# Kernel optimization log

Measured on AMD Instinct MI355X. Metric: run time of the kernel, lower is better.

## Reference

```python
import jax, jax.numpy as jnp
import numpy as np

N = 50000        # nodes
E = 1600000      # edges (avg degree 32)
DIM_IN = 128
H = 4            # num_heads
D1 = 100         # gc1 per-head out dim
D2 = 20          # gc2 per-head out dim
B = 64           # graphs in the batch
EPS = 1e-5
SLOPE = 0.01     # torch leaky_relu default


def setup_inputs() -> dict:
    key = jax.random.key(0)
    ks = jax.random.split(key, 16)
    sc = lambda fan: 1.0 / np.sqrt(fan)
    inp = {
        'feat': jax.random.normal(ks[0], (N, DIM_IN), jnp.float32),
        'src': jax.random.randint(ks[1], (E,), 0, N, jnp.int32),
        'dst': jax.random.randint(ks[2], (E,), 0, N, jnp.int32),
        'graph_id': jnp.sort(jax.random.randint(ks[3], (N,), 0, B, jnp.int32)),
        # GAT layer 1: per-head fc weight [H, din, dout], attn vector [H, 2*dout]
        'W1': jax.random.normal(ks[4], (H, DIM_IN, D1), jnp.float32) * sc(DIM_IN),
        'a1': jax.random.normal(ks[5], (H, 2 * D1), jnp.float32) * sc(2 * D1),
        # GAT layer 2 (input is cat of heads: H*D1 = 400)
        'W2': jax.random.normal(ks[6], (H, H * D1, D2), jnp.float32) * sc(H * D1),
        'a2': jax.random.normal(ks[7], (H, 2 * D2), jnp.float32) * sc(2 * D2),
        # readout MLP 20 -> 128 -> 32 -> 1
        'Wf1': jax.random.normal(ks[8], (D2, 128), jnp.float32) * sc(D2),
        'bf1': jnp.zeros((128,), jnp.float32),
        'Wf2': jax.random.normal(ks[9], (128, 32), jnp.float32) * sc(128),
        'bf2': jnp.zeros((32,), jnp.float32),
        'Wf3': jax.random.normal(ks[10], (32, 1), jnp.float32) * sc(32),
        'bf3': jnp.zeros((1,), jnp.float32),
        'gamma2': jnp.ones((32,), jnp.float32),   # bn2 weight
        'beta2': jnp.zeros((32,), jnp.float32),   # bn2 bias
    }
    return inp


def _gat_heads(h, W, a, src, dst):
    """Per-head GAT: gather-attn -> segment softmax over dst mailboxes -> scatter-sum.
    Returns list of [N, dout] head outputs. Loop over H=4 heads (small fixed set)."""
    outs = []
    for i in range(W.shape[0]):
        z = h @ W[i]                               # [N, dout]
        d = z.shape[1]
        s_src = z @ a[i, :d]                       # [N] (attn split: a.[z_src,z_dst])
        s_dst = z @ a[i, d:]                       # [N]
        e = jax.nn.leaky_relu(s_src[src] + s_dst[dst], SLOPE)   # [E]
        m = jax.ops.segment_max(e, dst, num_segments=N)          # stable softmax max
        ex = jnp.exp(e - m[dst])
        den = jax.ops.segment_sum(ex, dst, num_segments=N)
        alpha = ex / den[dst]                      # [E] segment softmax
        outs.append(jax.ops.segment_sum(alpha[:, None] * z[src], dst, num_segments=N))
    return outs


def reference(feat, src, dst, graph_id, W1, a1, W2, a2,
              Wf1, bf1, Wf2, bf2, Wf3, bf3, gamma2, beta2):
    src = src.astype(jnp.int32); dst = dst.astype(jnp.int32)
    h = jax.nn.relu(jnp.concatenate(_gat_heads(feat, W1, a1, src, dst), axis=1))  # [N,400]
    h = jax.nn.relu(jnp.mean(jnp.stack(_gat_heads(h, W2, a2, src, dst), 0), 0))   # [N,20]
    # dgl.mean_nodes: per-graph mean of node features
    counts = jax.ops.segment_sum(jnp.ones((N,), h.dtype), graph_id, num_segments=B)
    hg = jax.ops.segment_sum(h, graph_id, num_segments=B) / counts[:, None]        # [B,20]
    out = jax.nn.relu(hg @ Wf1 + bf1)              # dropout = identity (eval)
    out = out @ Wf2 + bf2                          # [B,32]
    mu = jnp.mean(out, axis=0)                     # BatchNorm1d (training stats, biased var)
    var = jnp.mean((out - mu) ** 2, axis=0)
    out = jax.nn.relu(gamma2 * (out - mu) * jax.lax.rsqrt(var + EPS) + beta2)
    return out @ Wf3 + bf3                         # [B,1]
```

## Files before the change

kernel.cpp:

```cpp
#include <hip/hip_runtime.h>
#include <hip/hip_bf16.h>
#include <math.h>

#define N_NODES 50000
#define N_EDGES 1600000
#define DIN 128
#define NH 4
#define D1 100
#define D2 20
#define NB 64
#define EPS_BN 1e-5f


typedef unsigned int uint;
typedef unsigned short ushort;
typedef short short8v __attribute__((ext_vector_type(8)));
typedef float float4v __attribute__((ext_vector_type(4)));

#define Z1_ROWU 224
#define Z1_HU 52
#define Z2_ROWU 64

__device__ __forceinline__ void bf16x2_unpack(uint p, float& lo, float& hi) {
  lo = __uint_as_float(p << 16);
  hi = __uint_as_float(p & 0xffff0000u);
}

__device__ __forceinline__ ushort f2bf(float f) {
  uint u = __float_as_uint(f);
  return (ushort)((u + 0x7fffu + ((u >> 16) & 1u)) >> 16);
}

__global__ void prep_b1t(const float* __restrict__ W1, ushort* __restrict__ B1t) {
  int o = blockIdx.x * 256 + threadIdx.x;
  int h = o >> 14;
  int r = o & 16383;
  int j = r >> 7, k = r & 127;
  float v = (j < D1) ? W1[((size_t)h * DIN + k) * D1 + j] : 0.f;
  B1t[o] = f2bf(v);
}

__global__ void prep_b2t(const float* __restrict__ W2, ushort* __restrict__ B2t) {
  int idx = blockIdx.x * 256 + threadIdx.x;
  if (idx >= 80 * 416) return;
  int c = idx / 416, k = idx - c * 416;
  int h = c / D2, j = c - h * D2;
  float v = (k < NH * D1) ? W2[((size_t)h * (NH * D1) + k) * D2 + j] : 0.f;
  B2t[idx] = f2bf(v);
}

__global__ __launch_bounds__(256) void gemm1_mfma(const float* __restrict__ feat,
                                                  const ushort* __restrict__ B1t,
                                                  ushort* __restrict__ z1b) {
  __shared__ __align__(16) short As[64 * 136];
  __shared__ __align__(16) short Bs[128 * 136];
  const int row0 = blockIdx.x * 64;
  const int h = blockIdx.y;
  const int tid = threadIdx.x;
#pragma unroll
  for (int it = 0; it < 8; it++) {
    int idx = tid + it * 256;
    int r = idx >> 5, c4 = idx & 31;
    int row = row0 + r;
    float4 v = make_float4(0.f, 0.f, 0.f, 0.f);
    if (row < N_NODES) v = *reinterpret_cast<const float4*>(feat + (size_t)row * DIN + c4 * 4);
    short4 s;
    s.x = (short)f2bf(v.x); s.y = (short)f2bf(v.y);
    s.z = (short)f2bf(v.z); s.w = (short)f2bf(v.w);
    *reinterpret_cast<short4*>(&As[r * 136 + c4 * 4]) = s;
  }
  {
    const uint* bsrc = reinterpret_cast<const uint*>(B1t + (size_t)h * 16384);
#pragma unroll
    for (int it = 0; it < 32; it++) {
      int idx = tid + it * 256;
      int j = idx >> 6, kk = idx & 63;
      *reinterpret_cast<uint*>(&Bs[j * 136 + kk * 2]) = bsrc[idx];
    }
  }
  __syncthreads();
  const int wv = tid >> 6, lane = tid & 63;
  const int m = lane & 15, q = lane >> 4;
  float4v acc[8];
#pragma unroll
  for (int t = 0; t < 8; t++) acc[t] = (float4v){0.f, 0.f, 0.f, 0.f};
#pragma unroll
  for (int kq = 0; kq < 4; kq++) {
    short8v a = *reinterpret_cast<const short8v*>(&As[(wv * 16 + m) * 136 + kq * 32 + q * 8]);
#pragma unroll
    for (int t = 0; t < 8; t++) {
      short8v b = *reinterpret_cast<const short8v*>(&Bs[(t * 16 + m) * 136 + kq * 32 + q * 8]);
      acc[t] = __builtin_amdgcn_mfma_f32_16x16x32_bf16(a, b, acc[t], 0, 0, 0);
    }
  }
#pragma unroll
  for (int t = 0; t < 8; t++) {
    int cl = t * 16 + m;
    if (cl < 104) {
#pragma unroll
      for (int reg = 0; reg < 4; reg++) {
        int row = row0 + wv * 16 + q * 4 + reg;
        if (row < N_NODES)
          z1b[(size_t)row * 448 + h * 104 + cl] = (cl < D1) ? f2bf(acc[t][reg]) : (ushort)0;
      }
    }
  }
}

__global__ __launch_bounds__(256) void gemm2_mfma(const ushort* __restrict__ h1b,
                                                  const ushort* __restrict__ B2t,
                                                  ushort* __restrict__ z2b) {
  __shared__ __align__(16) short As[64 * 40];
  __shared__ __align__(16) short Bs[80 * 40];
  const int row0 = blockIdx.x * 64;
  const int tid = threadIdx.x;
  const int wv = tid >> 6, lane = tid & 63;
  const int m = lane & 15, q = lane >> 4;
  const uint* au = reinterpret_cast<const uint*>(h1b);
  const uint* bu = reinterpret_cast<const uint*>(B2t);
  uint* asu = reinterpret_cast<uint*>(As);
  uint* bsu = reinterpret_cast<uint*>(Bs);
  float4v acc[5];
#pragma unroll
  for (int t = 0; t < 5; t++) acc[t] = (float4v){0.f, 0.f, 0.f, 0.f};
  for (int ch = 0; ch < 13; ch++) {
    int k0u = ch * 16;
    {
      int idx = tid;
#pragma unroll
      for (int it = 0; it < 4; it++, idx += 256) {
        int r = idx >> 4, ku = idx & 15;
        int row = row0 + r;
        uint v = 0;
        if (row < N_NODES && (k0u + ku) < 200) v = au[(size_t)row * 200 + k0u + ku];
        asu[r * 20 + ku] = v;
      }
      idx = tid;
#pragma unroll
      for (int it = 0; it < 5; it++, idx += 256) {
        int c = idx >> 4, ku = idx & 15;
        bsu[c * 20 + ku] = bu[(size_t)c * 208 + k0u + ku];
      }
    }
    __syncthreads();
    short8v a = *reinterpret_cast<const short8v*>(&As[(wv * 16 + m) * 40 + q * 8]);
#pragma unroll
    for (int t = 0; t < 5; t++) {
      short8v b = *reinterpret_cast<const short8v*>(&Bs[(t * 16 + m) * 40 + q * 8]);
      acc[t] = __builtin_amdgcn_mfma_f32_16x16x32_bf16(a, b, acc[t], 0, 0, 0);
    }
    __syncthreads();
  }
#pragma unroll
  for (int t = 0; t < 5; t++) {
    int col = t * 16 + m;
#pragma unroll
    for (int reg = 0; reg < 4; reg++) {
      int row = row0 + wv * 16 + q * 4 + reg;
      if (row < N_NODES) z2b[(size_t)row * 128 + col] = f2bf(acc[t][reg]);
    }
  }
}

template <int DOUT, int HEADU, int ROWU>
__global__ void scores_kernel(const ushort* __restrict__ z,
                              const float* __restrict__ a,
                              float* __restrict__ ssrc,
                              float* __restrict__ sdst) {
  int t = blockIdx.x * blockDim.x + threadIdx.x;
  if (t >= N_NODES * NH) return;
  int n = t >> 2;
  int h = t & 3;
  const uint* zr = reinterpret_cast<const uint*>(z) + (size_t)n * ROWU + h * HEADU;
  const float* as = a + h * 2 * DOUT;
  const float* ad = as + DOUT;
  float s1 = 0.f, s2 = 0.f;
  for (int j = 0; j < DOUT / 2; j++) {
    float lo, hi;
    bf16x2_unpack(zr[j], lo, hi);
    s1 += lo * as[2 * j] + hi * as[2 * j + 1];
    s2 += lo * ad[2 * j] + hi * ad[2 * j + 1];
  }
  ssrc[h * N_NODES + n] = s1;
  sdst[h * N_NODES + n] = s2;
}

__global__ void hist_kernel(const int* __restrict__ dst, int* __restrict__ cnt) {
  int e = blockIdx.x * blockDim.x + threadIdx.x;
  if (e < N_EDGES) atomicAdd(&cnt[dst[e]], 1);
}

__global__ __launch_bounds__(512) void scan1_kernel(const int* __restrict__ cnt,
                                                    int* __restrict__ row_ptr,
                                                    int* __restrict__ btot, int n) {
  __shared__ int ws[8];
  int b = blockIdx.x, tid = threadIdx.x, lane = tid & 63, wv = tid >> 6;
  int i = b * 512 + tid;
  int v = (i < n) ? cnt[i] : 0;
  int orig = v;
  for (int off = 1; off < 64; off <<= 1) {
    int t = __shfl_up(v, off);
    if (lane >= off) v += t;
  }
  if (lane == 63) ws[wv] = v;
  __syncthreads();
  int wo = 0;
  for (int j = 0; j < wv; j++) wo += ws[j];
  if (i < n) row_ptr[i] = wo + v - orig;
  if (tid == 511) btot[b] = wo + v;
}

__global__ __launch_bounds__(128) void scan2_kernel(int* __restrict__ btot,
                                                    int* __restrict__ row_ptr_n, int nb) {
  __shared__ int ws2[2];
  int tid = threadIdx.x, lane = tid & 63, wv = tid >> 6;
  int v = (tid < nb) ? btot[tid] : 0;
  int orig = v;
  for (int off = 1; off < 64; off <<= 1) {
    int t = __shfl_up(v, off);
    if (lane >= off) v += t;
  }
  if (lane == 63) ws2[wv] = v;
  __syncthreads();
  int wo = (wv == 1) ? ws2[0] : 0;
  if (tid < nb) btot[tid] = wo + v - orig;
  if (tid == nb - 1) *row_ptr_n = wo + v;
}

__global__ __launch_bounds__(512) void scan3_kernel(int* __restrict__ row_ptr,
                                                    int* __restrict__ cursor,
                                                    const int* __restrict__ btot, int n) {
  int i = blockIdx.x * 512 + threadIdx.x;
  if (i < n) {
    int v = row_ptr[i] + btot[blockIdx.x];
    row_ptr[i] = v;
    cursor[i] = v;
  }
}

__global__ void fill_kernel(const int* __restrict__ src, const int* __restrict__ dst,
                            int* __restrict__ cursor, int* __restrict__ csr_src) {
  int e = blockIdx.x * blockDim.x + threadIdx.x;
  if (e < N_EDGES) {
    int p = atomicAdd(&cursor[dst[e]], 1);
    csr_src[p] = src[e];
  }
}

__global__ __launch_bounds__(256) void agg1_kernel(const ushort* __restrict__ z,
                                                   const float* __restrict__ ssrc,
                                                   const float* __restrict__ sdst,
                                                   const int* __restrict__ row_ptr,
                                                   const int* __restrict__ csr_src,
                                                   ushort* __restrict__ h1b) {
  __shared__ float lw[NH][128];
  const int d = blockIdx.x;
  const int h = threadIdx.x >> 6, lane = threadIdx.x & 63;
  const int beg = row_ptr[d], end = row_ptr[d + 1];
  const int deg = end - beg;
  uint* h1u = reinterpret_cast<uint*>(h1b);
  const size_t ou = (size_t)d * 200 + h * 50 + lane;
  const bool act = lane < D1 / 2;
  if (deg == 0) {
    if (act) h1u[ou] = 0u;
    return;
  }
  const int hN = h * N_NODES;
  const float sd = sdst[hN + d];
  const uint* zb = reinterpret_cast<const uint*>(z);
  const int hco = h * Z1_HU + lane;
  float den = 0.f;
  float aE0 = 0.f, aE1 = 0.f, aE2 = 0.f, aE3 = 0.f;
  float aO0 = 0.f, aO1 = 0.f, aO2 = 0.f, aO3 = 0.f;
  for (int c0 = 0; c0 < deg; c0 += 128) {
    const int cn = min(128, deg - c0);
    const int cb = beg + c0;
    for (int i = lane; i < cn; i += 64) {
      int s = csr_src[cb + i];
      float e = ssrc[hN + s] + sd;
      e = fmaxf(e, 0.01f * e);
      float x = __expf(e);
      lw[h][i] = x;
      den += x;
    }
    if (act) {
      int j = 0;
      for (; j + 8 <= cn; j += 8) {
        int s0 = csr_src[cb + j + 0], s1 = csr_src[cb + j + 1];
        int s2 = csr_src[cb + j + 2], s3 = csr_src[cb + j + 3];
        int s4 = csr_src[cb + j + 4], s5 = csr_src[cb + j + 5];
        int s6 = csr_src[cb + j + 6], s7 = csr_src[cb + j + 7];
        float x0 = lw[h][j + 0], x1 = lw[h][j + 1];
        float x2 = lw[h][j + 2], x3 = lw[h][j + 3];
        float x4 = lw[h][j + 4], x5 = lw[h][j + 5];
        float x6 = lw[h][j + 6], x7 = lw[h][j + 7];
        uint p0 = zb[(size_t)s0 * Z1_ROWU + hco];
        uint p1 = zb[(size_t)s1 * Z1_ROWU + hco];
        uint p2 = zb[(size_t)s2 * Z1_ROWU + hco];
        uint p3 = zb[(size_t)s3 * Z1_ROWU + hco];
        uint p4 = zb[(size_t)s4 * Z1_ROWU + hco];
        uint p5 = zb[(size_t)s5 * Z1_ROWU + hco];
        uint p6 = zb[(size_t)s6 * Z1_ROWU + hco];
        uint p7 = zb[(size_t)s7 * Z1_ROWU + hco];
        float lo, hi;
        bf16x2_unpack(p0, lo, hi); aE0 += x0 * lo; aO0 += x0 * hi;
        bf16x2_unpack(p1, lo, hi); aE1 += x1 * lo; aO1 += x1 * hi;
        bf16x2_unpack(p2, lo, hi); aE2 += x2 * lo; aO2 += x2 * hi;
        bf16x2_unpack(p3, lo, hi); aE3 += x3 * lo; aO3 += x3 * hi;
        bf16x2_unpack(p4, lo, hi); aE0 += x4 * lo; aO0 += x4 * hi;
        bf16x2_unpack(p5, lo, hi); aE1 += x5 * lo; aO1 += x5 * hi;
        bf16x2_unpack(p6, lo, hi); aE2 += x6 * lo; aO2 += x6 * hi;
        bf16x2_unpack(p7, lo, hi); aE3 += x7 * lo; aO3 += x7 * hi;
      }
      for (; j < cn; j++) {
        int s = csr_src[cb + j];
        float x = lw[h][j];
        uint p = zb[(size_t)s * Z1_ROWU + hco];
        float lo, hi;
        bf16x2_unpack(p, lo, hi);
        aE0 += x * lo;
        aO0 += x * hi;
      }
    }
  }
#pragma unroll
  for (int off = 32; off > 0; off >>= 1) den += __shfl_xor(den, off);
  if (!act) return;
  float inv = 1.0f / den;
  float vE = ((aE0 + aE1) + (aE2 + aE3)) * inv;
  float vO = ((aO0 + aO1) + (aO2 + aO3)) * inv;
  vE = vE > 0.f ? vE : 0.f;
  vO = vO > 0.f ? vO : 0.f;
  h1u[ou] = (uint)f2bf(vE) | ((uint)f2bf(vO) << 16);
}

__global__ __launch_bounds__(256) void agg2_kernel(const ushort* __restrict__ z,
                                                   const float* __restrict__ ssrc,
                                                   const float* __restrict__ sdst,
                                                   const int* __restrict__ row_ptr,
                                                   const int* __restrict__ csr_src,
                                                   float* __restrict__ h2) {
  __shared__ float xw[4][8][4];
  __shared__ int sw[4][8];
  __shared__ float accb[4][40][2];
  __shared__ float denb[4][4];
  const int d = blockIdx.x;
  const int wv = threadIdx.x >> 6, lane = threadIdx.x & 63;
  const int beg = row_ptr[d];
  const int deg = row_ptr[d + 1] - beg;
  if (deg == 0) {
    if (threadIdx.x < D2) h2[(size_t)d * D2 + threadIdx.x] = 0.f;
    return;
  }
  const int eh_h = lane & 3, eh_e = lane >> 2;
  const int hq = lane / 10;
  const uint* zu = reinterpret_cast<const uint*>(z);
  float sd = 0.f;
  if (lane < 32) sd = sdst[eh_h * N_NODES + d];
  float den = 0.f;
  float acc0 = 0.f, acc1 = 0.f;
  for (int c0 = wv * 8; c0 < deg; c0 += 32) {
    const int cn = min(8, deg - c0);
    const int cb = beg + c0;
    if (lane < 32) {
      int ee = (eh_e < cn) ? eh_e : 0;
      int s = csr_src[cb + ee];
      float e = ssrc[eh_h * N_NODES + s] + sd;
      e = fmaxf(e, 0.01f * e);
      float x = (eh_e < cn) ? __expf(e) : 0.f;
      den += x;
      xw[wv][eh_e][eh_h] = x;
      if (eh_h == 0) sw[wv][eh_e] = s;
    }
    if (lane < 40) {
#pragma unroll
      for (int e = 0; e < 8; e++) {
        int se = sw[wv][e];
        float xx = xw[wv][e][hq];
        uint p = zu[(size_t)se * Z2_ROWU + lane];
        float lo, hi;
        bf16x2_unpack(p, lo, hi);
        acc0 += xx * lo;
        acc1 += xx * hi;
      }
    }
  }
  den += __shfl_xor(den, 4);
  den += __shfl_xor(den, 8);
  den += __shfl_xor(den, 16);
  if (lane < 4) denb[wv][lane] = den;
  if (lane < 40) {
    accb[wv][lane][0] = acc0;
    accb[wv][lane][1] = acc1;
  }
  __syncthreads();
  if (threadIdx.x < 10) {
    int j = threadIdx.x;
    float vE = 0.f, vO = 0.f;
#pragma unroll
    for (int h = 0; h < 4; h++) {
      float dn = denb[0][h] + denb[1][h] + denb[2][h] + denb[3][h];
      float invd = 1.0f / dn;
      int sl = h * 10 + j;
      float lo = accb[0][sl][0] + accb[1][sl][0] + accb[2][sl][0] + accb[3][sl][0];
      float hi = accb[0][sl][1] + accb[1][sl][1] + accb[2][sl][1] + accb[3][sl][1];
      vE += lo * invd;
      vO += hi * invd;
    }
    vE *= 0.25f;
    vO *= 0.25f;
    h2[(size_t)d * D2 + 2 * j] = vE > 0.f ? vE : 0.f;
    h2[(size_t)d * D2 + 2 * j + 1] = vO > 0.f ? vO : 0.f;
  }
}

__global__ __launch_bounds__(256) void pool_kernel(const float* __restrict__ h2,
                                                   const int* __restrict__ gid,
                                                   float* __restrict__ hg,
                                                   int* __restrict__ gcnt) {
  int wave = threadIdx.x >> 6, lane = threadIdx.x & 63;
  int n = (blockIdx.x * 4 + wave) * 64 + lane;
  bool valid = n < N_NODES;
  int g = gid[valid ? n : (N_NODES - 1)];
  int g0 = __shfl(g, 0), g63 = __shfl(g, 63);
  unsigned long long mask = __ballot(valid);
  if (g0 == g63) {
    if (lane == 0) atomicAdd(&gcnt[g0], (int)__popcll(mask));
#pragma unroll
    for (int c = 0; c < D2; c++) {
      float v = valid ? h2[(size_t)n * D2 + c] : 0.f;
#pragma unroll
      for (int off = 32; off > 0; off >>= 1) v += __shfl_xor(v, off);
      if (lane == 0) atomicAdd(&hg[g0 * D2 + c], v);
    }
  } else if (valid) {
    atomicAdd(&gcnt[g], 1);
    for (int c = 0; c < D2; c++) atomicAdd(&hg[g * D2 + c], h2[(size_t)n * D2 + c]);
  }
}

__global__ __launch_bounds__(256) void head_kernel(const float* __restrict__ hg,
                                                   const int* __restrict__ gcnt,
                                                   const float* __restrict__ Wf1,
                                                   const float* __restrict__ bf1,
                                                   const float* __restrict__ Wf2,
                                                   const float* __restrict__ bf2,
                                                   const float* __restrict__ Wf3,
                                                   const float* __restrict__ bf3,
                                                   const float* __restrict__ gamma,
                                                   const float* __restrict__ beta,
                                                   float* __restrict__ out) {
  __shared__ float X[NB][D2];
  __shared__ float T1[NB][128];
  __shared__ float T2[NB][32];
  __shared__ float scale_s[32], shift_s[32];
  int tid = threadIdx.x;
  for (int i = tid; i < NB * D2; i += 256) {
    int r = i / D2, c = i % D2;
    X[r][c] = hg[i] / (float)gcnt[r];
  }
  __syncthreads();
  for (int i = tid; i < NB * 128; i += 256) {
    int r = i >> 7, c = i & 127;
    float s = bf1[c];
#pragma unroll
    for (int k = 0; k < D2; k++) s += X[r][k] * Wf1[k * 128 + c];
    T1[r][c] = s > 0.f ? s : 0.f;
  }
  __syncthreads();
  for (int i = tid; i < NB * 32; i += 256) {
    int r = i >> 5, c = i & 31;
    float s = bf2[c];
#pragma unroll
    for (int k = 0; k < 128; k++) s += T1[r][k] * Wf2[k * 32 + c];
    T2[r][c] = s;
  }
  __syncthreads();
  if (tid < 32) {
    float mu = 0.f;
    for (int r = 0; r < NB; r++) mu += T2[r][tid];
    mu *= (1.f / NB);
    float var = 0.f;
    for (int r = 0; r < NB; r++) {
      float dv = T2[r][tid] - mu;
      var += dv * dv;
    }
    var *= (1.f / NB);
    float sc = gamma[tid] * rsqrtf(var + EPS_BN);
    scale_s[tid] = sc;
    shift_s[tid] = beta[tid] - mu * sc;
  }
  __syncthreads();
  if (tid < NB) {
    float s = bf3[0];
#pragma unroll
    for (int c = 0; c < 32; c++) {
      float y = scale_s[c] * T2[tid][c] + shift_s[c];
      y = y > 0.f ? y : 0.f;
      s += y * Wf3[c];
    }
    out[tid] = s;
  }
}


extern "C" void kernel_launch(void* const* d_in, const int* in_sizes, int n_in,
                              void* d_out, int out_size, void* d_ws, size_t ws_size,
                              hipStream_t stream) {
  const float* feat = (const float*)d_in[0];
  const int* src = (const int*)d_in[1];
  const int* dst = (const int*)d_in[2];
  const int* gid = (const int*)d_in[3];
  const float* W1 = (const float*)d_in[4];
  const float* a1 = (const float*)d_in[5];
  const float* W2 = (const float*)d_in[6];
  const float* a2 = (const float*)d_in[7];
  const float* Wf1 = (const float*)d_in[8];
  const float* bf1 = (const float*)d_in[9];
  const float* Wf2 = (const float*)d_in[10];
  const float* bf2 = (const float*)d_in[11];
  const float* Wf3 = (const float*)d_in[12];
  const float* bf3 = (const float*)d_in[13];
  const float* gamma2 = (const float*)d_in[14];
  const float* beta2 = (const float*)d_in[15];
  float* outp = (float*)d_out;

  char* p = (char*)d_ws;
  auto alloc = [&](size_t bytes) {
    void* q = (void*)p;
    p += (bytes + 255) & ~(size_t)255;
    return q;
  };
  ushort* z1b = (ushort*)alloc((size_t)N_NODES * 448 * 2);
  ushort* z2b = (ushort*)alloc((size_t)N_NODES * 128 * 2);
  ushort* h1b = (ushort*)alloc((size_t)N_NODES * NH * D1 * 2);
  float* h2 = (float*)alloc((size_t)N_NODES * D2 * 4);
  float* ssrc = (float*)alloc((size_t)NH * N_NODES * 4);
  float* sdst = (float*)alloc((size_t)NH * N_NODES * 4);
  int* cnt = (int*)alloc((size_t)N_NODES * 4);
  int* row_ptr = (int*)alloc((size_t)(N_NODES + 1) * 4);
  int* cursor = (int*)alloc((size_t)N_NODES * 4);
  int* csr = (int*)alloc((size_t)N_EDGES * 4);
  int* btot = (int*)alloc((size_t)128 * 4);
  ushort* B1t = (ushort*)alloc((size_t)NH * 128 * 128 * 2);
  ushort* B2t = (ushort*)alloc((size_t)80 * 416 * 2);
  float* hg = (float*)alloc((size_t)NB * D2 * 4);
  int* gcnt = (int*)alloc((size_t)NB * 4);

  const int rows64 = (N_NODES + 63) / 64;
  const int eblk = (N_EDGES + 255) / 256;
  const int nblk = (N_NODES + 255) / 256;
  const int nhblk = (N_NODES * NH + 255) / 256;
  const int sblk = (N_NODES + 511) / 512;

  hipMemsetAsync(cnt, 0, (size_t)N_NODES * 4, stream);
  hist_kernel<<<eblk, 256, 0, stream>>>(dst, cnt);
  scan1_kernel<<<sblk, 512, 0, stream>>>(cnt, row_ptr, btot, N_NODES);
  scan2_kernel<<<1, 128, 0, stream>>>(btot, row_ptr + N_NODES, sblk);
  scan3_kernel<<<sblk, 512, 0, stream>>>(row_ptr, cursor, btot, N_NODES);
  fill_kernel<<<eblk, 256, 0, stream>>>(src, dst, cursor, csr);

  prep_b1t<<<256, 256, 0, stream>>>(W1, B1t);
  prep_b2t<<<130, 256, 0, stream>>>(W2, B2t);

  gemm1_mfma<<<dim3(rows64, NH), 256, 0, stream>>>(feat, B1t, z1b);
  scores_kernel<D1, Z1_HU, Z1_ROWU><<<nhblk, 256, 0, stream>>>(z1b, a1, ssrc, sdst);
  agg1_kernel<<<N_NODES, 256, 0, stream>>>(z1b, ssrc, sdst, row_ptr, csr, h1b);

  gemm2_mfma<<<rows64, 256, 0, stream>>>(h1b, B2t, z2b);
  scores_kernel<D2, 10, Z2_ROWU><<<nhblk, 256, 0, stream>>>(z2b, a2, ssrc, sdst);
  agg2_kernel<<<N_NODES, 256, 0, stream>>>(z2b, ssrc, sdst, row_ptr, csr, h2);

  hipMemsetAsync(hg, 0, (size_t)NB * D2 * 4, stream);
  hipMemsetAsync(gcnt, 0, (size_t)NB * 4, stream);
  pool_kernel<<<nblk, 256, 0, stream>>>(h2, gid, hg, gcnt);
  head_kernel<<<1, 256, 0, stream>>>(hg, gcnt, Wf1, bf1, Wf2, bf2, Wf3, bf3,
                                     gamma2, beta2, outp);
}
```

Baseline: 733.0 us.

## Record edge ranks in histogram, shrink z1 row stride, retile gemm1 to 128 rows

After: 631.2 us. 1.16x faster.

```diff
diff --git a/kernel.cpp b/kernel.cpp
--- a/kernel.cpp
+++ b/kernel.cpp
@@ -17,7 +17,7 @@
 typedef short short8v __attribute__((ext_vector_type(8)));
 typedef float float4v __attribute__((ext_vector_type(4)));
 
-#define Z1_ROWU 224
+#define Z1_ROWU 208
 #define Z1_HU 52
 #define Z2_ROWU 64
 
@@ -52,23 +52,10 @@
 __global__ __launch_bounds__(256) void gemm1_mfma(const float* __restrict__ feat,
                                                   const ushort* __restrict__ B1t,
                                                   ushort* __restrict__ z1b) {
-  __shared__ __align__(16) short As[64 * 136];
   __shared__ __align__(16) short Bs[128 * 136];
-  const int row0 = blockIdx.x * 64;
+  const int row0 = blockIdx.x * 128;
   const int h = blockIdx.y;
   const int tid = threadIdx.x;
-#pragma unroll
-  for (int it = 0; it < 8; it++) {
-    int idx = tid + it * 256;
-    int r = idx >> 5, c4 = idx & 31;
-    int row = row0 + r;
-    float4 v = make_float4(0.f, 0.f, 0.f, 0.f);
-    if (row < N_NODES) v = *reinterpret_cast<const float4*>(feat + (size_t)row * DIN + c4 * 4);
-    short4 s;
-    s.x = (short)f2bf(v.x); s.y = (short)f2bf(v.y);
-    s.z = (short)f2bf(v.z); s.w = (short)f2bf(v.w);
-    *reinterpret_cast<short4*>(&As[r * 136 + c4 * 4]) = s;
-  }
   {
     const uint* bsrc = reinterpret_cast<const uint*>(B1t + (size_t)h * 16384);
 #pragma unroll
@@ -78,30 +65,55 @@
       *reinterpret_cast<uint*>(&Bs[j * 136 + kk * 2]) = bsrc[idx];
     }
   }
-  __syncthreads();
   const int wv = tid >> 6, lane = tid & 63;
   const int m = lane & 15, q = lane >> 4;
-  float4v acc[8];
-#pragma unroll
-  for (int t = 0; t < 8; t++) acc[t] = (float4v){0.f, 0.f, 0.f, 0.f};
+  short8v a[2][4];
+#pragma unroll
+  for (int mt = 0; mt < 2; mt++) {
+    int row = row0 + wv * 32 + mt * 16 + m;
+    bool ok = row < N_NODES;
+    const float* fr = feat + (size_t)(ok ? row : 0) * DIN;
+#pragma unroll
+    for (int kq = 0; kq < 4; kq++) {
+      short8v s = (short8v){0, 0, 0, 0, 0, 0, 0, 0};
+      if (ok) {
+        float4 v0 = *reinterpret_cast<const float4*>(fr + kq * 32 + q * 8);
+        float4 v1 = *reinterpret_cast<const float4*>(fr + kq * 32 + q * 8 + 4);
+        s[0] = (short)f2bf(v0.x); s[1] = (short)f2bf(v0.y);
+        s[2] = (short)f2bf(v0.z); s[3] = (short)f2bf(v0.w);
+        s[4] = (short)f2bf(v1.x); s[5] = (short)f2bf(v1.y);
+        s[6] = (short)f2bf(v1.z); s[7] = (short)f2bf(v1.w);
+      }
+      a[mt][kq] = s;
+    }
+  }
+  __syncthreads();
+  float4v acc[2][8];
+#pragma unroll
+  for (int mt = 0; mt < 2; mt++)
+#pragma unroll
+    for (int t = 0; t < 8; t++) acc[mt][t] = (float4v){0.f, 0.f, 0.f, 0.f};
 #pragma unroll
   for (int kq = 0; kq < 4; kq++) {
-    short8v a = *reinterpret_cast<const short8v*>(&As[(wv * 16 + m) * 136 + kq * 32 + q * 8]);
 #pragma unroll
     for (int t = 0; t < 8; t++) {
       short8v b = *reinterpret_cast<const short8v*>(&Bs[(t * 16 + m) * 136 + kq * 32 + q * 8]);
-      acc[t] = __builtin_amdgcn_mfma_f32_16x16x32_bf16(a, b, acc[t], 0, 0, 0);
-    }
-  }
-#pragma unroll
-  for (int t = 0; t < 8; t++) {
-    int cl = t * 16 + m;
-    if (cl < 104) {
-#pragma unroll
-      for (int reg = 0; reg < 4; reg++) {
-        int row = row0 + wv * 16 + q * 4 + reg;
-        if (row < N_NODES)
-          z1b[(size_t)row * 448 + h * 104 + cl] = (cl < D1) ? f2bf(acc[t][reg]) : (ushort)0;
+      acc[0][t] = __builtin_amdgcn_mfma_f32_16x16x32_bf16(a[0][kq], b, acc[0][t], 0, 0, 0);
+      acc[1][t] = __builtin_amdgcn_mfma_f32_16x16x32_bf16(a[1][kq], b, acc[1][t], 0, 0, 0);
+    }
+  }
+#pragma unroll
+  for (int mt = 0; mt < 2; mt++) {
+#pragma unroll
+    for (int t = 0; t < 8; t++) {
+      int cl = t * 16 + m;
+      if (cl < 104) {
+#pragma unroll
+        for (int reg = 0; reg < 4; reg++) {
+          int row = row0 + wv * 32 + mt * 16 + q * 4 + reg;
+          if (row < N_NODES)
+            z1b[(size_t)row * 416 + h * 104 + cl] = (cl < D1) ? f2bf(acc[mt][t][reg]) : (ushort)0;
+        }
       }
     }
   }
@@ -185,9 +197,10 @@
   sdst[h * N_NODES + n] = s2;
 }
 
-__global__ void hist_kernel(const int* __restrict__ dst, int* __restrict__ cnt) {
+__global__ void hist_kernel(const int* __restrict__ dst, int* __restrict__ cnt,
+                            int* __restrict__ rank) {
   int e = blockIdx.x * blockDim.x + threadIdx.x;
-  if (e < N_EDGES) atomicAdd(&cnt[dst[e]], 1);
+  if (e < N_EDGES) rank[e] = atomicAdd(&cnt[dst[e]], 1);
 }
 
 __global__ __launch_bounds__(512) void scan1_kernel(const int* __restrict__ cnt,
@@ -228,23 +241,16 @@
 }
 
 __global__ __launch_bounds__(512) void scan3_kernel(int* __restrict__ row_ptr,
-                                                    int* __restrict__ cursor,
                                                     const int* __restrict__ btot, int n) {
   int i = blockIdx.x * 512 + threadIdx.x;
-  if (i < n) {
-    int v = row_ptr[i] + btot[blockIdx.x];
-    row_ptr[i] = v;
-    cursor[i] = v;
-  }
+  if (i < n) row_ptr[i] += btot[blockIdx.x];
 }
 
 __global__ void fill_kernel(const int* __restrict__ src, const int* __restrict__ dst,
-                            int* __restrict__ cursor, int* __restrict__ csr_src) {
+                            const int* __restrict__ row_ptr, const int* __restrict__ rank,
+                            int* __restrict__ csr_src) {
   int e = blockIdx.x * blockDim.x + threadIdx.x;
-  if (e < N_EDGES) {
-    int p = atomicAdd(&cursor[dst[e]], 1);
-    csr_src[p] = src[e];
-  }
+  if (e < N_EDGES) csr_src[row_ptr[dst[e]] + rank[e]] = src[e];
 }
 
 __global__ __launch_bounds__(256) void agg1_kernel(const ushort* __restrict__ z,
@@ -531,7 +537,7 @@
     p += (bytes + 255) & ~(size_t)255;
     return q;
   };
-  ushort* z1b = (ushort*)alloc((size_t)N_NODES * 448 * 2);
+  ushort* z1b = (ushort*)alloc((size_t)N_NODES * 416 * 2);
   ushort* z2b = (ushort*)alloc((size_t)N_NODES * 128 * 2);
   ushort* h1b = (ushort*)alloc((size_t)N_NODES * NH * D1 * 2);
   float* h2 = (float*)alloc((size_t)N_NODES * D2 * 4);
@@ -539,7 +545,7 @@
   float* sdst = (float*)alloc((size_t)NH * N_NODES * 4);
   int* cnt = (int*)alloc((size_t)N_NODES * 4);
   int* row_ptr = (int*)alloc((size_t)(N_NODES + 1) * 4);
-  int* cursor = (int*)alloc((size_t)N_NODES * 4);
+  int* rank = (int*)alloc((size_t)N_EDGES * 4);
   int* csr = (int*)alloc((size_t)N_EDGES * 4);
   int* btot = (int*)alloc((size_t)128 * 4);
   ushort* B1t = (ushort*)alloc((size_t)NH * 128 * 128 * 2);
@@ -547,6 +553,7 @@
   float* hg = (float*)alloc((size_t)NB * D2 * 4);
   int* gcnt = (int*)alloc((size_t)NB * 4);
 
+  const int rows128 = (N_NODES + 127) / 128;
   const int rows64 = (N_NODES + 63) / 64;
   const int eblk = (N_EDGES + 255) / 256;
   const int nblk = (N_NODES + 255) / 256;
@@ -554,16 +561,16 @@
   const int sblk = (N_NODES + 511) / 512;
 
   hipMemsetAsync(cnt, 0, (size_t)N_NODES * 4, stream);
-  hist_kernel<<<eblk, 256, 0, stream>>>(dst, cnt);
+  hist_kernel<<<eblk, 256, 0, stream>>>(dst, cnt, rank);
   scan1_kernel<<<sblk, 512, 0, stream>>>(cnt, row_ptr, btot, N_NODES);
   scan2_kernel<<<1, 128, 0, stream>>>(btot, row_ptr + N_NODES, sblk);
-  scan3_kernel<<<sblk, 512, 0, stream>>>(row_ptr, cursor, btot, N_NODES);
-  fill_kernel<<<eblk, 256, 0, stream>>>(src, dst, cursor, csr);
+  scan3_kernel<<<sblk, 512, 0, stream>>>(row_ptr, btot, N_NODES);
+  fill_kernel<<<eblk, 256, 0, stream>>>(src, dst, row_ptr, rank, csr);
 
   prep_b1t<<<256, 256, 0, stream>>>(W1, B1t);
   prep_b2t<<<130, 256, 0, stream>>>(W2, B2t);
 
-  gemm1_mfma<<<dim3(rows64, NH), 256, 0, stream>>>(feat, B1t, z1b);
+  gemm1_mfma<<<dim3(rows128, NH), 256, 0, stream>>>(feat, B1t, z1b);
   scores_kernel<D1, Z1_HU, Z1_ROWU><<<nhblk, 256, 0, stream>>>(z1b, a1, ssrc, sdst);
   agg1_kernel<<<N_NODES, 256, 0, stream>>>(z1b, ssrc, sdst, row_ptr, csr, h1b);
 
```
